# Optimization experiments

Measured on AMD Instinct MI355X. Metric: run time of the kernel, lower is better.

The kernel has to match this reference:

```python
import jax, jax.numpy as jnp
import numpy as np

N_NODES = 50000
N_EDGES = 1600000
IN_CH = 128
HEADS = 4
OUT_CH = 32
NEG_SLOPE = 0.2
EPS = 1e-9


def setup_inputs() -> dict:
    key = jax.random.key(0)
    k_x, k_ei, k_w, k_as, k_ad = jax.random.split(key, 5)
    x = jax.random.normal(k_x, (N_NODES, IN_CH), dtype=jnp.float32)
    edge_index = jax.random.randint(k_ei, (2, N_EDGES), 0, N_NODES, dtype=jnp.int64)
    # xavier-uniform-like init for params
    wb = np.sqrt(6.0 / (IN_CH + HEADS * OUT_CH))
    weight = jax.random.uniform(k_w, (IN_CH, HEADS * OUT_CH), minval=-wb, maxval=wb, dtype=jnp.float32)
    ab = np.sqrt(6.0 / (HEADS + OUT_CH))
    att_src = jax.random.uniform(k_as, (HEADS, OUT_CH), minval=-ab, maxval=ab, dtype=jnp.float32)
    att_dst = jax.random.uniform(k_ad, (HEADS, OUT_CH), minval=-ab, maxval=ab, dtype=jnp.float32)
    bias = jnp.zeros((HEADS * OUT_CH,), dtype=jnp.float32)
    return {"x": x, "edge_index": edge_index, "weight": weight,
            "att_src": att_src, "att_dst": att_dst, "bias": bias}


def reference(x, edge_index, weight, att_src, att_dst, bias):
    N = x.shape[0]
    H, C = att_src.shape
    # add self loops
    loop = jnp.arange(N, dtype=edge_index.dtype)
    ei = jnp.concatenate([edge_index, jnp.stack([loop, loop], axis=0)], axis=1)
    src, dst = ei[0], ei[1]
    # linear projection -> [N, H, C]
    h = (x @ weight).reshape(N, H, C)
    # per-node attention logits, then gather per edge (same math as gathering h first)
    a_s = jnp.einsum('nhc,hc->nh', h, att_src)  # [N, H]
    a_d = jnp.einsum('nhc,hc->nh', h, att_dst)  # [N, H]
    scores = a_s[src] + a_d[dst]                # [E, H]
    scores = jnp.where(scores >= 0, scores, NEG_SLOPE * scores)  # leaky_relu
    # edge softmax over incoming edges of each dst node (all heads vectorized)
    mx = jax.ops.segment_max(scores, dst, num_segments=N)        # [N, H]
    ex = jnp.exp(scores - mx[dst])                               # [E, H]
    denom = jax.ops.segment_sum(ex, dst, num_segments=N)         # [N, H]
    alpha = ex / (denom[dst] + EPS)                              # [E, H]
    # weighted scatter-add aggregation
    msgs = alpha[:, :, None] * h[src]                            # [E, H, C]
    agg = jax.ops.segment_sum(msgs, dst, num_segments=N)         # [N, H, C]
    out = agg.reshape(N, H * C) + bias
    return out
```

## Files before the change

### kernel.cpp

```cpp
#include <hip/hip_runtime.h>

#define NN 50000
#define NE 1600000
#define IN_CH 128
#define HEADS 4
#define OUT_CH 32
#define HC 128
#define NEG_SLOPE 0.2f
#define EPS 1e-9f
#define SEG 96

#define FGRP 8
#define DPG (NN / FGRP)
#define FILL_BPG ((NE / 8 + 255) / 256)
#define ROWS_PB 64
#define PROJ_BLOCKS ((NN + ROWS_PB - 1) / ROWS_PB)
#define XPITCH 136
#define INIT_BLOCKS ((NN + 255) / 256)
#define GMAX_BLOCKS ((NN + 255) / 256)

#define ENC_NEG_INF 0x007FFFFFu

using bf16x8 = __attribute__((ext_vector_type(8))) short;
using f32x4  = __attribute__((ext_vector_type(4))) float;
using u16x8  = __attribute__((ext_vector_type(8))) unsigned short;

__device__ __forceinline__ float leaky(float v) {
    return v >= 0.0f ? v : NEG_SLOPE * v;
}
__device__ __forceinline__ unsigned short f2bf(float f) {
    unsigned u = __float_as_uint(f);
    return (unsigned short)((u + 0x7fffu + ((u >> 16) & 1u)) >> 16);
}
__device__ __forceinline__ float bf2f(unsigned short b) {
    return __uint_as_float((unsigned)b << 16);
}
__device__ __forceinline__ unsigned int fenc(float f) {
    unsigned int u = __float_as_uint(f);
    return (u & 0x80000000u) ? ~u : (u | 0x80000000u);
}
__device__ __forceinline__ float fdec(unsigned int u) {
    return (u & 0x80000000u) ? __uint_as_float(u & 0x7fffffffu)
                             : __uint_as_float(~u);
}

__global__ __launch_bounds__(256) void k_init(int* __restrict__ cnt,
                                              unsigned int* __restrict__ gmax,
                                              const float* __restrict__ W,
                                              unsigned short* __restrict__ Wt_bf) {
    int i = blockIdx.x * 256 + threadIdx.x;
    if (i < HEADS) gmax[i] = ENC_NEG_INF;
    if (i < NN) cnt[i] = 0;
    if (i < IN_CH * HC) {
        int k = i >> 7, n = i & 127;
        Wt_bf[n * IN_CH + k] = f2bf(W[i]);
    }
}

__global__ __launch_bounds__(256) void k_proj_fill(
        const float* __restrict__ x,
        const unsigned short* __restrict__ Wt_bf,
        const float* __restrict__ att_s, const float* __restrict__ att_d,
        unsigned short* __restrict__ h_bf,
        float* __restrict__ a_s, float* __restrict__ a_d,
        const int* __restrict__ ei, int* __restrict__ cnt,
        unsigned short* __restrict__ csr_src) {
    if (blockIdx.x >= PROJ_BLOCKS) {
        const int fb = blockIdx.x - PROJ_BLOCKS;
        const int f = fb & (FGRP - 1);
        const int bg = fb >> 3;
        const int e0 = (bg * 256 + (int)threadIdx.x) * 8;
        if (e0 >= NE) return;
        const int lo = f * DPG;
        const int4 d0 = *(const int4*)(ei + NE + e0);
        const int4 d1 = *(const int4*)(ei + NE + e0 + 4);
        const int4 s0 = *(const int4*)(ei + e0);
        const int4 s1 = *(const int4*)(ei + e0 + 4);
        const int d[8] = {d0.x, d0.y, d0.z, d0.w, d1.x, d1.y, d1.z, d1.w};
        const int s[8] = {s0.x, s0.y, s0.z, s0.w, s1.x, s1.y, s1.z, s1.w};
#pragma unroll
        for (int k = 0; k < 8; ++k) {
            if ((unsigned)(d[k] - lo) < (unsigned)DPG) {
                const int pos = atomicAdd(&cnt[d[k]], 1);
                if (pos < SEG)
                    csr_src[(size_t)d[k] * SEG + pos] = (unsigned short)s[k];
            }
        }
        return;
    }
    __shared__ short xs[ROWS_PB * XPITCH];
    const int tid = threadIdx.x;
    const int n0 = blockIdx.x * ROWS_PB;

#pragma unroll
    for (int it = 0; it < 8; ++it) {
        const int idx = it * 256 + tid;
        const int row = idx >> 5;
        const int k4 = idx & 31;
        float4 v = make_float4(0.f, 0.f, 0.f, 0.f);
        if (n0 + row < NN) v = *(const float4*)(x + (size_t)(n0 + row) * IN_CH + k4 * 4);
        short* p = &xs[row * XPITCH + k4 * 4];
        p[0] = (short)f2bf(v.x); p[1] = (short)f2bf(v.y);
        p[2] = (short)f2bf(v.z); p[3] = (short)f2bf(v.w);
    }
    __syncthreads();

    const int wave = tid >> 6;
    const int lane = tid & 63;
    const int quad = lane >> 4;
    const int m16 = lane & 15;
    const int wrow = wave * 16;

    bf16x8 a[4];
#pragma unroll
    for (int ks = 0; ks < 4; ++ks)
        a[ks] = *(const bf16x8*)&xs[(wrow + m16) * XPITCH + ks * 32 + quad * 8];

    const int row_base = n0 + wrow + quad * 4;
#pragma unroll
    for (int hh = 0; hh < 4; ++hh) {
        float psh[4] = {0.f, 0.f, 0.f, 0.f};
        float pdh[4] = {0.f, 0.f, 0.f, 0.f};
#pragma unroll
        for (int c2 = 0; c2 < 2; ++c2) {
            const int ct = hh * 2 + c2;
            const unsigned short* wb = Wt_bf + (size_t)(ct * 16 + m16) * IN_CH + quad * 8;
            bf16x8 b0 = *(const bf16x8*)(wb);
            bf16x8 b1 = *(const bf16x8*)(wb + 32);
            bf16x8 b2 = *(const bf16x8*)(wb + 64);
            bf16x8 b3 = *(const bf16x8*)(wb + 96);
            f32x4 acc = {0.f, 0.f, 0.f, 0.f};
            acc = __builtin_amdgcn_mfma_f32_16x16x32_bf16(a[0], b0, acc, 0, 0, 0);
            acc = __builtin_amdgcn_mfma_f32_16x16x32_bf16(a[1], b1, acc, 0, 0, 0);
            acc = __builtin_amdgcn_mfma_f32_16x16x32_bf16(a[2], b2, acc, 0, 0, 0);
            acc = __builtin_amdgcn_mfma_f32_16x16x32_bf16(a[3], b3, acc, 0, 0, 0);
            const int col = ct * 16 + m16;
            const float asv = att_s[col];
            const float adv = att_d[col];
#pragma unroll
            for (int r = 0; r < 4; ++r) {
                const int n = row_base + r;
                if (n < NN) h_bf[(size_t)n * HC + col] = f2bf(acc[r]);
                psh[r] = fmaf(acc[r], asv, psh[r]);
                pdh[r] = fmaf(acc[r], adv, pdh[r]);
            }
        }
#pragma unroll
        for (int mk = 1; mk <= 8; mk <<= 1) {
#pragma unroll
            for (int r = 0; r < 4; ++r) {
                psh[r] += __shfl_xor(psh[r], mk, 64);
                pdh[r] += __shfl_xor(pdh[r], mk, 64);
            }
        }
        if (m16 == 0) {
#pragma unroll
            for (int r = 0; r < 4; ++r) {
                const int n = row_base + r;
                if (n < NN) {
                    a_s[n * HEADS + hh] = psh[r];
                    a_d[n * HEADS + hh] = pdh[r];
                }
            }
        }
    }
}

__global__ __launch_bounds__(256) void k_gmax(const float* __restrict__ a_s,
                                              unsigned int* __restrict__ gmax) {
    const int n = blockIdx.x * 256 + threadIdx.x;
    float4 m4 = make_float4(-1e30f, -1e30f, -1e30f, -1e30f);
    if (n < NN) m4 = *(const float4*)(a_s + n * 4);
#pragma unroll
    for (int m = 32; m >= 1; m >>= 1) {
        m4.x = fmaxf(m4.x, __shfl_xor(m4.x, m, 64));
        m4.y = fmaxf(m4.y, __shfl_xor(m4.y, m, 64));
        m4.z = fmaxf(m4.z, __shfl_xor(m4.z, m, 64));
        m4.w = fmaxf(m4.w, __shfl_xor(m4.w, m, 64));
    }
    __shared__ float wm[4][4];
    const int wv = threadIdx.x >> 6;
    if ((threadIdx.x & 63) == 0) {
        wm[wv][0] = m4.x; wm[wv][1] = m4.y; wm[wv][2] = m4.z; wm[wv][3] = m4.w;
    }
    __syncthreads();
    if (threadIdx.x < 4) {
        float mm = fmaxf(fmaxf(wm[0][threadIdx.x], wm[1][threadIdx.x]),
                         fmaxf(wm[2][threadIdx.x], wm[3][threadIdx.x]));
        atomicMax(&gmax[threadIdx.x], fenc(mm));
    }
}

__global__ __launch_bounds__(256) void k_agg(const int* __restrict__ cnt,
                                             const unsigned short* __restrict__ csr_src,
                                             const unsigned short* __restrict__ h_bf,
                                             const float* __restrict__ a_s,
                                             const float* __restrict__ a_d,
                                             const unsigned int* __restrict__ gmax,
                                             const float* __restrict__ bias,
                                             float* __restrict__ out) {
    const int n = blockIdx.x * 4 + (threadIdx.x >> 6);
    const int lane = threadIdx.x & 63;
    if (n >= NN) return;
    const int q = lane >> 4;
    const int ql = lane & 15;
    const int hd = ql >> 2;
    int dg = cnt[n];
    if (dg > SEG) dg = SEG;
    const int beg = n * SEG;
    const int end = beg + dg;

    const float ad_h = a_d[n * 4 + hd];
    const float bound = leaky(fdec(gmax[hd]) + ad_h);

    float ev = 0.25f * __expf(leaky(a_s[n * 4 + hd] + ad_h) - bound);
    float denom = ev;
    const u16x8 hs = *(const u16x8*)(h_bf + (size_t)n * HC + 8 * ql);
    float acc[8];
#pragma unroll
    for (int k = 0; k < 8; ++k) acc[k] = ev * bf2f(hs[k]);

    int i = beg + q;
    int s0v = (i < end)     ? (int)csr_src[i]     : n;
    int s1v = (i + 4 < end) ? (int)csr_src[i + 4] : n;
    float as0 = a_s[s0v * 4 + hd];
    u16x8 hv0 = *(const u16x8*)(h_bf + (size_t)s0v * HC + 8 * ql);

    for (; i < end; i += 4) {
        const int s2v = (i + 8 < end) ? (int)csr_src[i + 8] : n;
        const float as1 = a_s[s1v * 4 + hd];
        const u16x8 hv1 = *(const u16x8*)(h_bf + (size_t)s1v * HC + 8 * ql);
        const float e = __expf(leaky(as0 + ad_h) - bound);
        denom += e;
#pragma unroll
        for (int k = 0; k < 8; ++k)
            acc[k] = fmaf(e, bf2f(hv0[k]), acc[k]);
        as0 = as1; hv0 = hv1; s1v = s2v;
    }
#pragma unroll
    for (int k = 0; k < 8; ++k) {
        acc[k] += __shfl_xor(acc[k], 16, 64);
        acc[k] += __shfl_xor(acc[k], 32, 64);
    }
    denom += __shfl_xor(denom, 16, 64);
    denom += __shfl_xor(denom, 32, 64);

    if (q == 0) {
        const float inv = 1.0f / (denom + EPS);
        float* o = out + (size_t)n * HC + 8 * ql;
        const float* b = bias + 8 * ql;
        f32x4 o0, o1;
        o0[0] = acc[0] * inv + b[0]; o0[1] = acc[1] * inv + b[1];
        o0[2] = acc[2] * inv + b[2]; o0[3] = acc[3] * inv + b[3];
        o1[0] = acc[4] * inv + b[4]; o1[1] = acc[5] * inv + b[5];
        o1[2] = acc[6] * inv + b[6]; o1[3] = acc[7] * inv + b[7];
        __builtin_nontemporal_store(o0, (f32x4*)(o));
        __builtin_nontemporal_store(o1, (f32x4*)(o + 4));
    }
}

extern "C" void kernel_launch(void* const* d_in, const int* in_sizes, int n_in,
                              void* d_out, int out_size, void* d_ws, size_t ws_size,
                              hipStream_t stream) {
    const float* x     = (const float*)d_in[0];
    const int*   ei    = (const int*)d_in[1];
    const float* W     = (const float*)d_in[2];
    const float* att_s = (const float*)d_in[3];
    const float* att_d = (const float*)d_in[4];
    const float* bias  = (const float*)d_in[5];
    float* out = (float*)d_out;

    char* ws = (char*)d_ws;
    int*   cnt     = (int*)ws;    ws += (size_t)NN * 4;
    unsigned int* gmax = (unsigned int*)ws; ws += 64;
    unsigned short* csr_src = (unsigned short*)ws; ws += (size_t)NN * SEG * 2;
    unsigned short* h_bf = (unsigned short*)ws; ws += (size_t)NN * HC * 2;
    float* a_s     = (float*)ws;  ws += (size_t)NN * HEADS * 4;
    float* a_d     = (float*)ws;  ws += (size_t)NN * HEADS * 4;
    unsigned short* Wt_bf = (unsigned short*)ws; ws += (size_t)IN_CH * HC * 2;

    k_init     <<<INIT_BLOCKS, 256, 0, stream>>>(cnt, gmax, W, Wt_bf);
    k_proj_fill<<<PROJ_BLOCKS + FGRP * FILL_BPG, 256, 0, stream>>>(
        x, Wt_bf, att_s, att_d, h_bf, a_s, a_d, ei, cnt, csr_src);
    k_gmax     <<<GMAX_BLOCKS, 256, 0, stream>>>(a_s, gmax);
    k_agg      <<<(NN + 3) / 4, 256, 0, stream>>>(cnt, csr_src, h_bf, a_s, a_d,
                                                  gmax, bias, out);
}
```

Measured before the change: 220.1 us.

## Fuse all stages into one persistent cooperative kernel with grid syncs

Replaces the four separate kernel launches (init, projection+CSR fill, global max, aggregation) with a single cooperative kernel. It runs 1536 persistent blocks that loop over each stage's logical blocks and separate the stages with grid-wide syncs. The goal is to remove launch gaps and the tail drain between kernels. The risks are the cost of grid.sync, reduced occupancy from launch bounds and shared LDS in the fused kernel, and the grid-stride scheduling being less balanced. If the cooperative launch fails, it falls back to the old multi-kernel path.

```diff
diff --git a/kernel.cpp b/kernel.cpp
--- a/kernel.cpp
+++ b/kernel.cpp
@@ -1,4 +1,6 @@
 #include <hip/hip_runtime.h>
+#include <hip/hip_cooperative_groups.h>
+namespace cg = cooperative_groups;
 
 #define NN 50000
 #define NE 1600000
@@ -13,11 +15,16 @@
 #define FGRP 8
 #define DPG (NN / FGRP)
 #define FILL_BPG ((NE / 8 + 255) / 256)
+#define FILL_LB (FGRP * FILL_BPG)
 #define ROWS_PB 64
 #define PROJ_BLOCKS ((NN + ROWS_PB - 1) / ROWS_PB)
+#define P1_LB (PROJ_BLOCKS + FILL_LB)
 #define XPITCH 136
-#define INIT_BLOCKS ((NN + 255) / 256)
-#define GMAX_BLOCKS ((NN + 255) / 256)
+#define INIT_LB ((NN + 255) / 256)
+#define GMAX_LB ((NN + 255) / 256)
+#define AGG_LB ((NN + 3) / 4)
+
+#define GRID_BLKS 1536
 
 #define ENC_NEG_INF 0x007FFFFFu
 
@@ -44,11 +51,11 @@
                              : __uint_as_float(~u);
 }
 
-__global__ __launch_bounds__(256) void k_init(int* __restrict__ cnt,
-                                              unsigned int* __restrict__ gmax,
-                                              const float* __restrict__ W,
-                                              unsigned short* __restrict__ Wt_bf) {
-    int i = blockIdx.x * 256 + threadIdx.x;
+
+__device__ __forceinline__ void init_body(int b, int tid,
+        int* __restrict__ cnt, unsigned int* __restrict__ gmax,
+        const float* __restrict__ W, unsigned short* __restrict__ Wt_bf) {
+    const int i = b * 256 + tid;
     if (i < HEADS) gmax[i] = ENC_NEG_INF;
     if (i < NN) cnt[i] = 0;
     if (i < IN_CH * HC) {
@@ -57,41 +64,36 @@
     }
 }
 
-__global__ __launch_bounds__(256) void k_proj_fill(
-        const float* __restrict__ x,
-        const unsigned short* __restrict__ Wt_bf,
+__device__ __forceinline__ void fill_body(int fb, int tid,
+        const int* __restrict__ ei, int* __restrict__ cnt,
+        unsigned short* __restrict__ csr_src) {
+    const int f = fb & (FGRP - 1);
+    const int bg = fb >> 3;
+    const int e0 = (bg * 256 + tid) * 8;
+    if (e0 >= NE) return;
+    const int lo = f * DPG;
+    const int4 d0 = *(const int4*)(ei + NE + e0);
+    const int4 d1 = *(const int4*)(ei + NE + e0 + 4);
+    const int4 s0 = *(const int4*)(ei + e0);
+    const int4 s1 = *(const int4*)(ei + e0 + 4);
+    const int d[8] = {d0.x, d0.y, d0.z, d0.w, d1.x, d1.y, d1.z, d1.w};
+    const int s[8] = {s0.x, s0.y, s0.z, s0.w, s1.x, s1.y, s1.z, s1.w};
+#pragma unroll
+    for (int k = 0; k < 8; ++k) {
+        if ((unsigned)(d[k] - lo) < (unsigned)DPG) {
+            const int pos = atomicAdd(&cnt[d[k]], 1);
+            if (pos < SEG)
+                csr_src[(size_t)d[k] * SEG + pos] = (unsigned short)s[k];
+        }
+    }
+}
+
+__device__ __forceinline__ void proj_body(int b, int tid, short* xs,
+        const float* __restrict__ x, const unsigned short* __restrict__ Wt_bf,
         const float* __restrict__ att_s, const float* __restrict__ att_d,
         unsigned short* __restrict__ h_bf,
-        float* __restrict__ a_s, float* __restrict__ a_d,
-        const int* __restrict__ ei, int* __restrict__ cnt,
-        unsigned short* __restrict__ csr_src) {
-    if (blockIdx.x >= PROJ_BLOCKS) {
-        const int fb = blockIdx.x - PROJ_BLOCKS;
-        const int f = fb & (FGRP - 1);
-        const int bg = fb >> 3;
-        const int e0 = (bg * 256 + (int)threadIdx.x) * 8;
-        if (e0 >= NE) return;
-        const int lo = f * DPG;
-        const int4 d0 = *(const int4*)(ei + NE + e0);
-        const int4 d1 = *(const int4*)(ei + NE + e0 + 4);
-        const int4 s0 = *(const int4*)(ei + e0);
-        const int4 s1 = *(const int4*)(ei + e0 + 4);
-        const int d[8] = {d0.x, d0.y, d0.z, d0.w, d1.x, d1.y, d1.z, d1.w};
-        const int s[8] = {s0.x, s0.y, s0.z, s0.w, s1.x, s1.y, s1.z, s1.w};
-#pragma unroll
-        for (int k = 0; k < 8; ++k) {
-            if ((unsigned)(d[k] - lo) < (unsigned)DPG) {
-                const int pos = atomicAdd(&cnt[d[k]], 1);
-                if (pos < SEG)
-                    csr_src[(size_t)d[k] * SEG + pos] = (unsigned short)s[k];
-            }
-        }
-        return;
-    }
-    __shared__ short xs[ROWS_PB * XPITCH];
-    const int tid = threadIdx.x;
-    const int n0 = blockIdx.x * ROWS_PB;
-
+        float* __restrict__ a_s, float* __restrict__ a_d) {
+    const int n0 = b * ROWS_PB;
 #pragma unroll
     for (int it = 0; it < 8; ++it) {
         const int idx = it * 256 + tid;
@@ -164,11 +166,12 @@
             }
         }
     }
-}
-
-__global__ __launch_bounds__(256) void k_gmax(const float* __restrict__ a_s,
-                                              unsigned int* __restrict__ gmax) {
-    const int n = blockIdx.x * 256 + threadIdx.x;
+    __syncthreads();
+}
+
+__device__ __forceinline__ void gmax_body(int b, int tid, float (*wm)[4],
+        const float* __restrict__ a_s, unsigned int* __restrict__ gmax) {
+    const int n = b * 256 + tid;
     float4 m4 = make_float4(-1e30f, -1e30f, -1e30f, -1e30f);
     if (n < NN) m4 = *(const float4*)(a_s + n * 4);
 #pragma unroll
@@ -178,29 +181,27 @@
         m4.z = fmaxf(m4.z, __shfl_xor(m4.z, m, 64));
         m4.w = fmaxf(m4.w, __shfl_xor(m4.w, m, 64));
     }
-    __shared__ float wm[4][4];
-    const int wv = threadIdx.x >> 6;
-    if ((threadIdx.x & 63) == 0) {
+    const int wv = tid >> 6;
+    if ((tid & 63) == 0) {
         wm[wv][0] = m4.x; wm[wv][1] = m4.y; wm[wv][2] = m4.z; wm[wv][3] = m4.w;
     }
     __syncthreads();
-    if (threadIdx.x < 4) {
-        float mm = fmaxf(fmaxf(wm[0][threadIdx.x], wm[1][threadIdx.x]),
-                         fmaxf(wm[2][threadIdx.x], wm[3][threadIdx.x]));
-        atomicMax(&gmax[threadIdx.x], fenc(mm));
-    }
-}
-
-__global__ __launch_bounds__(256) void k_agg(const int* __restrict__ cnt,
-                                             const unsigned short* __restrict__ csr_src,
-                                             const unsigned short* __restrict__ h_bf,
-                                             const float* __restrict__ a_s,
-                                             const float* __restrict__ a_d,
-                                             const unsigned int* __restrict__ gmax,
-                                             const float* __restrict__ bias,
-                                             float* __restrict__ out) {
-    const int n = blockIdx.x * 4 + (threadIdx.x >> 6);
-    const int lane = threadIdx.x & 63;
+    if (tid < 4) {
+        float mm = fmaxf(fmaxf(wm[0][tid], wm[1][tid]),
+                         fmaxf(wm[2][tid], wm[3][tid]));
+        atomicMax(&gmax[tid], fenc(mm));
+    }
+    __syncthreads();
+}
+
+__device__ __forceinline__ void agg_body(int b, int tid,
+        const int* __restrict__ cnt, const unsigned short* __restrict__ csr_src,
+        const unsigned short* __restrict__ h_bf,
+        const float* __restrict__ a_s, const float* __restrict__ a_d,
+        const unsigned int* __restrict__ gmax,
+        const float* __restrict__ bias, float* __restrict__ out) {
+    const int n = b * 4 + (tid >> 6);
+    const int lane = tid & 63;
     if (n >= NN) return;
     const int q = lane >> 4;
     const int ql = lane & 15;
@@ -248,15 +249,85 @@
     if (q == 0) {
         const float inv = 1.0f / (denom + EPS);
         float* o = out + (size_t)n * HC + 8 * ql;
-        const float* b = bias + 8 * ql;
+        const float* bb = bias + 8 * ql;
         f32x4 o0, o1;
-        o0[0] = acc[0] * inv + b[0]; o0[1] = acc[1] * inv + b[1];
-        o0[2] = acc[2] * inv + b[2]; o0[3] = acc[3] * inv + b[3];
-        o1[0] = acc[4] * inv + b[4]; o1[1] = acc[5] * inv + b[5];
-        o1[2] = acc[6] * inv + b[6]; o1[3] = acc[7] * inv + b[7];
+        o0[0] = acc[0] * inv + bb[0]; o0[1] = acc[1] * inv + bb[1];
+        o0[2] = acc[2] * inv + bb[2]; o0[3] = acc[3] * inv + bb[3];
+        o1[0] = acc[4] * inv + bb[4]; o1[1] = acc[5] * inv + bb[5];
+        o1[2] = acc[6] * inv + bb[6]; o1[3] = acc[7] * inv + bb[7];
         __builtin_nontemporal_store(o0, (f32x4*)(o));
         __builtin_nontemporal_store(o1, (f32x4*)(o + 4));
     }
+}
+
+__global__ __launch_bounds__(256, 6) void k_fused(
+        const float* __restrict__ x, const int* __restrict__ ei,
+        const float* __restrict__ W,
+        const float* __restrict__ att_s, const float* __restrict__ att_d,
+        const float* __restrict__ bias, float* __restrict__ out,
+        int* __restrict__ cnt, unsigned int* __restrict__ gmax,
+        unsigned short* __restrict__ csr_src, unsigned short* __restrict__ h_bf,
+        float* __restrict__ a_s, float* __restrict__ a_d,
+        unsigned short* __restrict__ Wt_bf) {
+    cg::grid_group grid = cg::this_grid();
+    __shared__ short xs[ROWS_PB * XPITCH];
+    __shared__ float wm[4][4];
+    const int tid = threadIdx.x;
+
+    for (int b = blockIdx.x; b < INIT_LB; b += GRID_BLKS)
+        init_body(b, tid, cnt, gmax, W, Wt_bf);
+    grid.sync();
+
+    for (int b = blockIdx.x; b < P1_LB; b += GRID_BLKS) {
+        if (b >= PROJ_BLOCKS)
+            fill_body(b - PROJ_BLOCKS, tid, ei, cnt, csr_src);
+        else
+            proj_body(b, tid, xs, x, Wt_bf, att_s, att_d, h_bf, a_s, a_d);
+    }
+    grid.sync();
+
+    for (int b = blockIdx.x; b < GMAX_LB; b += GRID_BLKS)
+        gmax_body(b, tid, wm, a_s, gmax);
+    grid.sync();
+
+    for (int b = blockIdx.x; b < AGG_LB; b += GRID_BLKS)
+        agg_body(b, tid, cnt, csr_src, h_bf, a_s, a_d, gmax, bias, out);
+}
+
+__global__ __launch_bounds__(256) void k_init(int* __restrict__ cnt,
+        unsigned int* __restrict__ gmax, const float* __restrict__ W,
+        unsigned short* __restrict__ Wt_bf) {
+    init_body(blockIdx.x, threadIdx.x, cnt, gmax, W, Wt_bf);
+}
+
+__global__ __launch_bounds__(256) void k_proj_fill(
+        const float* __restrict__ x, const unsigned short* __restrict__ Wt_bf,
+        const float* __restrict__ att_s, const float* __restrict__ att_d,
+        unsigned short* __restrict__ h_bf,
+        float* __restrict__ a_s, float* __restrict__ a_d,
+        const int* __restrict__ ei, int* __restrict__ cnt,
+        unsigned short* __restrict__ csr_src) {
+    if (blockIdx.x >= PROJ_BLOCKS) {
+        fill_body(blockIdx.x - PROJ_BLOCKS, threadIdx.x, ei, cnt, csr_src);
+        return;
+    }
+    __shared__ short xs[ROWS_PB * XPITCH];
+    proj_body(blockIdx.x, threadIdx.x, xs, x, Wt_bf, att_s, att_d, h_bf, a_s, a_d);
+}
+
+__global__ __launch_bounds__(256) void k_gmax(const float* __restrict__ a_s,
+                                              unsigned int* __restrict__ gmax) {
+    __shared__ float wm[4][4];
+    gmax_body(blockIdx.x, threadIdx.x, wm, a_s, gmax);
+}
+
+__global__ __launch_bounds__(256) void k_agg(const int* __restrict__ cnt,
+        const unsigned short* __restrict__ csr_src,
+        const unsigned short* __restrict__ h_bf,
+        const float* __restrict__ a_s, const float* __restrict__ a_d,
+        const unsigned int* __restrict__ gmax,
+        const float* __restrict__ bias, float* __restrict__ out) {
+    agg_body(blockIdx.x, threadIdx.x, cnt, csr_src, h_bf, a_s, a_d, gmax, bias, out);
 }
 
 extern "C" void kernel_launch(void* const* d_in, const int* in_sizes, int n_in,
@@ -279,10 +350,20 @@
     float* a_d     = (float*)ws;  ws += (size_t)NN * HEADS * 4;
     unsigned short* Wt_bf = (unsigned short*)ws; ws += (size_t)IN_CH * HC * 2;
 
-    k_init     <<<INIT_BLOCKS, 256, 0, stream>>>(cnt, gmax, W, Wt_bf);
-    k_proj_fill<<<PROJ_BLOCKS + FGRP * FILL_BPG, 256, 0, stream>>>(
-        x, Wt_bf, att_s, att_d, h_bf, a_s, a_d, ei, cnt, csr_src);
-    k_gmax     <<<GMAX_BLOCKS, 256, 0, stream>>>(a_s, gmax);
-    k_agg      <<<(NN + 3) / 4, 256, 0, stream>>>(cnt, csr_src, h_bf, a_s, a_d,
-                                                  gmax, bias, out);
-}
+    void* args[] = {(void*)&x, (void*)&ei, (void*)&W, (void*)&att_s,
+                    (void*)&att_d, (void*)&bias, (void*)&out, (void*)&cnt,
+                    (void*)&gmax, (void*)&csr_src, (void*)&h_bf, (void*)&a_s,
+                    (void*)&a_d, (void*)&Wt_bf};
+    hipError_t err = hipLaunchCooperativeKernel((const void*)k_fused,
+                                                dim3(GRID_BLKS), dim3(256),
+                                                args, 0, stream);
+    if (err != hipSuccess) {
+        (void)hipGetLastError();
+        k_init     <<<INIT_LB, 256, 0, stream>>>(cnt, gmax, W, Wt_bf);
+        k_proj_fill<<<PROJ_BLOCKS + FILL_LB, 256, 0, stream>>>(
+            x, Wt_bf, att_s, att_d, h_bf, a_s, a_d, ei, cnt, csr_src);
+        k_gmax     <<<GMAX_LB, 256, 0, stream>>>(a_s, gmax);
+        k_agg      <<<AGG_LB, 256, 0, stream>>>(cnt, csr_src, h_bf, a_s, a_d,
+                                                gmax, bias, out);
+    }
+}
```

Result: slower. 696.2 us (+216.3%).
